# Optimization experiments

Measured on AMD Instinct MI355X. Metric: run time of the kernel, lower is better.

The kernel has to match this reference:

```python
import jax, jax.numpy as jnp
from jax import lax
import numpy as np

DN = ('NCHW', 'OIHW', 'NCHW')

def _conv(x, w, b, s, p):
    out = lax.conv_general_dilated(x, w, (s, s), ((p, p), (p, p)), dimension_numbers=DN)
    return out + b[None, :, None, None]

def _convt(x, w, b):
    # torch ConvTranspose2d(k=3, stride=2, pad=1, out_pad=1) == lhs-dilated conv
    # with flipped kernel, pad (k-1-p, k-1-p+op) = (1, 2). Doubles H, W.
    wk = jnp.flip(w, (2, 3)).transpose(1, 0, 2, 3)  # [Cin,Cout,k,k] -> [Cout,Cin,k,k]
    out = lax.conv_general_dilated(x, wk, (1, 1), ((1, 2), (1, 2)), lhs_dilation=(2, 2), dimension_numbers=DN)
    return out + b[None, :, None, None]

def _bn(x, g, b):
    # training-mode batch stats over (N, H, W), eps=1e-5
    m = jnp.mean(x, (0, 2, 3), keepdims=True)
    v = jnp.var(x, (0, 2, 3), keepdims=True)
    return (x - m) * lax.rsqrt(v + 1e-5) * g[None, :, None, None] + b[None, :, None, None]

def _hsw(x):
    return x * jnp.clip(x + 3.0, 0.0, 6.0) * (1.0 / 6.0)

SCORE_THRESHOLD = 0.6
DOWN_SCALE = 4.0

def _forward(feature, ch_w1, ch_b1, ch_w2, ch_b2, ch_w3, ch_b3, ch_g1, ch_be1, ch_g2, ch_be2,
             cl_w1, cl_b1, cl_w2, cl_b2, cl_g, cl_be, cl_dw, cl_db,
             rg_tw, rg_tb, rg_g, rg_be, rg_w, rg_b, hm_tw, hm_tb):
    # ---- CommonHead (note: original reuses bn1 after both stride-2 convs) ----
    h = _bn(_conv(feature, ch_w1, ch_b1, 2, 1), ch_g1, ch_be1)   # [B,192,64,64]
    h = _bn(_conv(h, ch_w2, ch_b2, 2, 1), ch_g1, ch_be1)         # [B,192,32,32]
    h = _hsw(_bn(_conv(h, ch_w3, ch_b3, 1, 0), ch_g2, ch_be2))   # [B,32,32,32]
    # ---- PageClassifyNet ----
    c = _hsw(_bn(_conv(h, cl_w1, cl_b1, 1, 1), cl_g, cl_be))     # [B,32,32,32]
    c = _conv(c, cl_w2, cl_b2, 1, 1)                             # [B,1,32,32]
    cls = c.reshape(c.shape[0], -1) @ cl_dw.T + cl_db            # [B,2]
    r = _hsw(_bn(_convt(feature, rg_tw, rg_tb), rg_g, rg_be))    # [B,32,256,256]
    reg = _conv(r, rg_w, rg_b, 1, 1)                             # [B,2,256,256]
    # ---- AuxiliaryHeatmapNet ----
    hm = _convt(feature, hm_tw, hm_tb)                           # [B,8,256,256]
    # ---- keypoint decode (threshold + argmax + gather), vectorized over batch ----
    B, _, H, W = hm.shape
    flat = hm.transpose(0, 2, 3, 1).reshape(B, H * W, 8)          # HWC layout as in source
    pages = jnp.stack([flat[..., :4], flat[..., 4:]], axis=1)     # [B,2(pages),HW,4(corners)]
    idx = jnp.argmax(pages, axis=2)                               # [B,2,4] flat spatial index
    y_idx = (idx // W).astype(reg.dtype)
    x_idx = (idx % W).astype(reg.dtype)
    fi = idx.reshape(B, -1)                                       # [B,8]
    reg_flat = reg.reshape(B, 2, H * W)
    off_x = jnp.take_along_axis(reg_flat[:, 0, :], fi, axis=1).reshape(B, 2, 4)
    off_y = jnp.take_along_axis(reg_flat[:, 1, :], fi, axis=1).reshape(B, 2, 4)
    xs = jnp.clip((off_x + x_idx) * DOWN_SCALE / (W * DOWN_SCALE), 0.0, 1.0)
    ys = jnp.clip((off_y + y_idx) * DOWN_SCALE / (H * DOWN_SCALE), 0.0, 1.0)
    valid = cls > SCORE_THRESHOLD                                 # [B,2]
    label = jnp.broadcast_to(jnp.arange(2, dtype=xs.dtype)[None, :], (B, 2))
    row = jnp.concatenate([label[..., None], xs, ys], axis=-1)    # [B,2,9]
    return jnp.where(valid[..., None], row, jnp.asarray(-1.0, xs.dtype))


def setup_inputs() -> dict:
    key = jax.random.key(0)
    ks = jax.random.split(key, 32)
    rn = lambda k, shp, s=0.05: jax.random.normal(k, shp, dtype=jnp.float32) * s
    d = {}
    d['feature'] = jax.random.normal(ks[0], (8, 512, 128, 128), dtype=jnp.float32)
    d['ch_w1'] = rn(ks[1], (192, 512, 3, 3)); d['ch_b1'] = rn(ks[2], (192,))
    d['ch_w2'] = rn(ks[3], (192, 192, 3, 3)); d['ch_b2'] = rn(ks[4], (192,))
    d['ch_w3'] = rn(ks[5], (32, 192, 1, 1)); d['ch_b3'] = rn(ks[6], (32,))
    d['ch_g1'] = jnp.ones((192,), jnp.float32); d['ch_be1'] = jnp.zeros((192,), jnp.float32)
    d['ch_g2'] = jnp.ones((32,), jnp.float32); d['ch_be2'] = jnp.zeros((32,), jnp.float32)
    d['cl_w1'] = rn(ks[7], (32, 32, 3, 3)); d['cl_b1'] = rn(ks[8], (32,))
    d['cl_w2'] = rn(ks[9], (1, 32, 3, 3)); d['cl_b2'] = rn(ks[10], (1,))
    d['cl_g'] = jnp.ones((32,), jnp.float32); d['cl_be'] = jnp.zeros((32,), jnp.float32)
    d['cl_dw'] = rn(ks[11], (2, 1024), 0.1); d['cl_db'] = rn(ks[12], (2,))
    d['rg_tw'] = rn(ks[13], (512, 32, 3, 3)); d['rg_tb'] = rn(ks[14], (32,))
    d['rg_g'] = jnp.ones((32,), jnp.float32); d['rg_be'] = jnp.zeros((32,), jnp.float32)
    d['rg_w'] = rn(ks[15], (2, 32, 3, 3)); d['rg_b'] = rn(ks[16], (2,))
    d['hm_tw'] = rn(ks[17], (512, 8, 3, 3)); d['hm_tb'] = rn(ks[18], (8,))
    return d


def reference(feature, ch_w1, ch_b1, ch_w2, ch_b2, ch_w3, ch_b3, ch_g1, ch_be1, ch_g2, ch_be2,
              cl_w1, cl_b1, cl_w2, cl_b2, cl_g, cl_be, cl_dw, cl_db,
              rg_tw, rg_tb, rg_g, rg_be, rg_w, rg_b, hm_tw, hm_tb):
    return _forward(feature, ch_w1, ch_b1, ch_w2, ch_b2, ch_w3, ch_b3, ch_g1, ch_be1, ch_g2, ch_be2,
                    cl_w1, cl_b1, cl_w2, cl_b2, cl_g, cl_be, cl_dw, cl_db,
                    rg_tw, rg_tb, rg_g, rg_be, rg_w, rg_b, hm_tw, hm_tb)
```

## Files before the change

### kernel.cpp

```cpp
#include <hip/hip_runtime.h>

typedef unsigned short u16;
typedef u16 u16x8 __attribute__((ext_vector_type(8)));
typedef __bf16 bf16x8 __attribute__((ext_vector_type(8)));
typedef float f32x4 __attribute__((ext_vector_type(4)));

__device__ __forceinline__ float bf2f(u16 v) {
  unsigned u = ((unsigned)v) << 16;
  return __builtin_bit_cast(float, u);
}
__device__ __forceinline__ u16 f2bf(float f) {
  unsigned u = __builtin_bit_cast(unsigned, f);
  u += 0x7FFFu + ((u >> 16) & 1u);
  return (u16)(u >> 16);
}
__device__ __forceinline__ float hsw(float v) {
  return v * fminf(fmaxf(v + 3.f, 0.f), 6.f) * (1.f / 6.f);
}
__device__ __forceinline__ f32x4 mfma16(u16x8 a, u16x8 b, f32x4 c) {
  return __builtin_amdgcn_mfma_f32_16x16x32_bf16(
      __builtin_bit_cast(bf16x8, a), __builtin_bit_cast(bf16x8, b), c, 0, 0, 0);
}

#define LR 40

__global__ __launch_bounds__(256) void k_tobf(const float* __restrict__ f,
                                              u16* __restrict__ fbh) {
  __shared__ float tl[64 * 65];
  const int t = threadIdx.x;
  const int bid = blockIdx.x;
  const int ict = bid & 7, xt = (bid >> 3) & 1, y = (bid >> 4) & 127, n = bid >> 11;
  const int x0 = xt * 64, ic0 = ict * 64;
#pragma unroll
  for (int i = 0; i < 16; ++i) {
    const int e = t + i * 256;
    const int icl = e >> 6, xl = e & 63;
    tl[icl * 65 + xl] = f[((n * 512 + ic0 + icl) * 128 + y) * 128 + x0 + xl];
  }
  __syncthreads();
#pragma unroll
  for (int i = 0; i < 16; ++i) {
    const int e = t + i * 256;
    const int xl = e >> 6, icl = e & 63;
    const size_t idx = ((size_t)((n * 128 + y) * 128 + x0 + xl) << 9) + ic0 + icl;
    fbh[idx] = f2bf(tl[icl * 65 + xl]);
  }
}

__global__ __launch_bounds__(256) void k_pack1(const float* __restrict__ w,
                                               u16* __restrict__ bph) {
  const int e = blockIdx.x * 256 + threadIdx.x;
  const int ici = e & 31;
  const int rest = e >> 5;
  const int oc = rest % 192;
  const int kc = rest / 192;
  const int icc = kc & 15, tap = kc >> 4;
  const int ic = icc * 32 + ici;
  bph[e] = f2bf(w[(oc * 512 + ic) * 9 + tap]);
}

__global__ __launch_bounds__(256) void k_pack2(const float* __restrict__ w,
                                               u16* __restrict__ bph) {
  const int e = blockIdx.x * 256 + threadIdx.x;
  const int ici = e & 31;
  const int rest = e >> 5;
  const int oc = rest % 192;
  const int kc = rest / 192;
  const int icc = kc % 6, tap = kc / 6;
  const int ic = icc * 32 + ici;
  bph[e] = f2bf(w[(oc * 192 + ic) * 9 + tap]);
}

__global__ __launch_bounds__(256) void k_pack5(const float* __restrict__ rgw,
                                               const float* __restrict__ hmw,
                                               u16* __restrict__ bph) {
  const int e = blockIdx.x * 256 + threadIdx.x;
  const int ici = e & 31;
  const int rest = e >> 5;
  const int oc = rest % 48;
  const int sic = rest / 48;
  const int icc = sic & 15, slot = sic >> 4;
  const int ic = icc * 32 + ici;
  const int kytab[9] = {1, 1, 1, 2, 0, 2, 2, 0, 0};
  const int kxtab[9] = {1, 2, 0, 1, 1, 2, 0, 2, 0};
  const int ky = kytab[slot], kx = kxtab[slot];
  float v = 0.f;
  if (oc < 32)
    v = rgw[((ic * 32 + oc) * 3 + ky) * 3 + kx];
  else if (oc < 40)
    v = hmw[((ic * 8 + (oc - 32)) * 3 + ky) * 3 + kx];
  bph[e] = f2bf(v);
}

__global__ __launch_bounds__(256) void k_conv1(const u16* __restrict__ fbh,
                                               const u16* __restrict__ bph,
                                               const float* __restrict__ bias,
                                               u16* __restrict__ y1) {
  __shared__ u16 Al[64 * LR];
  __shared__ u16 Bl[192 * LR];
  __shared__ float bl[192];
  const int t = threadIdx.x;
  const int n = blockIdx.x >> 6, oy = blockIdx.x & 63;
  if (t < 192) bl[t] = bias[t];
  const int lane = t & 63, wv = t >> 6;
  const int row = lane & 15, g = lane >> 4;
  const int oxs = t >> 2, icq = t & 3;
  const f32x4 z4 = {0.f, 0.f, 0.f, 0.f};
  f32x4 acc[4][3];
#pragma unroll
  for (int i = 0; i < 4; ++i)
#pragma unroll
    for (int j = 0; j < 3; ++j) acc[i][j] = z4;

#define C1_LOAD(KC, AV, BV)                                                    \
  {                                                                            \
    const int tap_ = (KC) >> 4, icc_ = (KC)&15;                                \
    const int ky_ = tap_ / 3, kx_ = tap_ - ky_ * 3;                            \
    const int iy_ = 2 * oy - 1 + ky_;                                          \
    const int ix_ = 2 * oxs - 1 + kx_;                                         \
    u16x8 v_ = {0, 0, 0, 0, 0, 0, 0, 0};                                       \
    if ((unsigned)iy_ < 128u && (unsigned)ix_ < 128u)                          \
      v_ = *(const u16x8*)&fbh[((size_t)((n * 128 + iy_) * 128 + ix_) << 9) +  \
                               icc_ * 32 + icq * 8];                           \
    AV = v_;                                                                   \
    const size_t bbase_ = (size_t)(tap_ * 16 + icc_) * (192 * 32);             \
    _Pragma("unroll") for (int i_ = 0; i_ < 3; ++i_) {                         \
      const int e_ = t + i_ * 256;                                             \
      BV[i_] = *(const u16x8*)&bph[bbase_ + (e_ >> 2) * 32 + (e_ & 3) * 8];    \
    }                                                                          \
  }

  u16x8 avA, bvA[3], avB, bvB[3];
  C1_LOAD(0, avA, bvA);

  for (int kc = 0; kc < 144; ++kc) {
    __syncthreads();
    *(u16x8*)&Al[oxs * LR + icq * 8] = avA;
#pragma unroll
    for (int i = 0; i < 3; ++i) {
      const int e = t + i * 256;
      *(u16x8*)&Bl[(e >> 2) * LR + (e & 3) * 8] = bvA[i];
    }
    __syncthreads();
    if (kc < 143) C1_LOAD(kc + 1, avB, bvB);
    u16x8 af[4], bf[3];
#pragma unroll
    for (int mf = 0; mf < 4; ++mf)
      af[mf] = *(const u16x8*)&Al[(mf * 16 + row) * LR + g * 8];
#pragma unroll
    for (int nf = 0; nf < 3; ++nf)
      bf[nf] = *(const u16x8*)&Bl[(wv * 48 + nf * 16 + row) * LR + g * 8];
#pragma unroll
    for (int mf = 0; mf < 4; ++mf)
#pragma unroll
      for (int nf = 0; nf < 3; ++nf) acc[mf][nf] = mfma16(af[mf], bf[nf], acc[mf][nf]);
    avA = avB;
#pragma unroll
    for (int i = 0; i < 3; ++i) bvA[i] = bvB[i];
  }
#undef C1_LOAD
#pragma unroll
  for (int mf = 0; mf < 4; ++mf)
#pragma unroll
    for (int nf = 0; nf < 3; ++nf)
#pragma unroll
      for (int r = 0; r < 4; ++r) {
        const int m = mf * 16 + g * 4 + r;
        const int oc = wv * 48 + nf * 16 + row;
        y1[((n * 64 + oy) * 64 + m) * 192 + oc] = f2bf(acc[mf][nf][r] + bl[oc]);
      }
}

__global__ __launch_bounds__(256) void k_conv2(const u16* __restrict__ y1,
                                               const u16* __restrict__ bph,
                                               const float* __restrict__ bias,
                                               const float* __restrict__ sc,
                                               const float* __restrict__ sh,
                                               float* __restrict__ y2) {
  __shared__ u16 Al[64 * LR];
  __shared__ u16 Bl[192 * LR];
  __shared__ float bl[192], scl[192], shl[192];
  const int t = threadIdx.x;
  const int n = blockIdx.x >> 4, oyp = blockIdx.x & 15;
  if (t < 192) {
    bl[t] = bias[t];
    scl[t] = sc[t];
    shl[t] = sh[t];
  }
  __syncthreads();
  const int lane = t & 63, wv = t >> 6;
  const int row = lane & 15, g = lane >> 4;
  const int ms = t >> 2, icq = t & 3;
  const int ryr = ms >> 5, oxs = ms & 31;
  const f32x4 z4 = {0.f, 0.f, 0.f, 0.f};
  f32x4 acc[4][3];
#pragma unroll
  for (int i = 0; i < 4; ++i)
#pragma unroll
    for (int j = 0; j < 3; ++j) acc[i][j] = z4;

#define C2_LOAD(KC, RAW, OK, BV)                                               \
  {                                                                            \
    const int tap_ = (KC) / 6, icc_ = (KC)-tap_ * 6;                           \
    const int ky_ = tap_ / 3, kx_ = tap_ - ky_ * 3;                            \
    const int iy_ = 2 * (oyp * 2 + ryr) - 1 + ky_;                             \
    const int ix_ = 2 * oxs - 1 + kx_;                                         \
    OK = ((unsigned)iy_ < 64u) && ((unsigned)ix_ < 64u);                       \
    u16x8 v_ = {0, 0, 0, 0, 0, 0, 0, 0};                                       \
    if (OK)                                                                    \
      v_ = *(const u16x8*)&y1[((n * 64 + iy_) * 64 + ix_) * 192 + icc_ * 32 +  \
                              icq * 8];                                        \
    RAW = v_;                                                                  \
    const size_t bbase_ = (size_t)(tap_ * 6 + icc_) * (192 * 32);              \
    _Pragma("unroll") for (int i_ = 0; i_ < 3; ++i_) {                         \
      const int e_ = t + i_ * 256;                                             \
      BV[i_] = *(const u16x8*)&bph[bbase_ + (e_ >> 2) * 32 + (e_ & 3) * 8];    \
    }                                                                          \
  }

  u16x8 rawA, bvA[3], rawB, bvB[3];
  bool okA, okB;
  C2_LOAD(0, rawA, okA, bvA);

  for (int kc = 0; kc < 54; ++kc) {
    const int tap = kc / 6, icc = kc - tap * 6;
    const int icb = icc * 32 + icq * 8;
    u16x8 av = {0, 0, 0, 0, 0, 0, 0, 0};
    if (okA) {
#pragma unroll
      for (int j = 0; j < 8; ++j)
        av[j] = f2bf(bf2f(rawA[j]) * scl[icb + j] + shl[icb + j]);
    }
    __syncthreads();
    *(u16x8*)&Al[ms * LR + icq * 8] = av;
#pragma unroll
    for (int i = 0; i < 3; ++i) {
      const int e = t + i * 256;
      *(u16x8*)&Bl[(e >> 2) * LR + (e & 3) * 8] = bvA[i];
    }
    __syncthreads();
    if (kc < 53) C2_LOAD(kc + 1, rawB, okB, bvB);
    u16x8 af[4], bf[3];
#pragma unroll
    for (int mf = 0; mf < 4; ++mf)
      af[mf] = *(const u16x8*)&Al[(mf * 16 + row) * LR + g * 8];
#pragma unroll
    for (int nf = 0; nf < 3; ++nf)
      bf[nf] = *(const u16x8*)&Bl[(wv * 48 + nf * 16 + row) * LR + g * 8];
#pragma unroll
    for (int mf = 0; mf < 4; ++mf)
#pragma unroll
      for (int nf = 0; nf < 3; ++nf) acc[mf][nf] = mfma16(af[mf], bf[nf], acc[mf][nf]);
    rawA = rawB;
    okA = okB;
#pragma unroll
    for (int i = 0; i < 3; ++i) bvA[i] = bvB[i];
  }
#undef C2_LOAD
#pragma unroll
  for (int mf = 0; mf < 4; ++mf)
#pragma unroll
    for (int nf = 0; nf < 3; ++nf)
#pragma unroll
      for (int r = 0; r < 4; ++r) {
        const int m = mf * 16 + g * 4 + r;
        const int oy = oyp * 2 + (m >> 5), ox = m & 31;
        const int oc = wv * 48 + nf * 16 + row;
        y2[((n * 32 + oy) * 32 + ox) * 192 + oc] = acc[mf][nf][r] + bl[oc];
      }
}

#define AST2 32
#define ARS2 (129 * 32)
__global__ __launch_bounds__(256) void k_convt(const u16* __restrict__ fbh,
                                               const u16* __restrict__ bph,
                                               const float* __restrict__ rgb,
                                               const float* __restrict__ hmb,
                                               u16* __restrict__ rr,
                                               float* __restrict__ hm) {
  __shared__ u16 AH[2 * ARS2];
  __shared__ u16 BH[9 * 48 * 32];
  const int t = threadIdx.x;
  const int bid = (blockIdx.x & 7) * 128 + (blockIdx.x >> 3);
  const int n = bid >> 7, iyb = bid & 127;
  const int lane = t & 63, wv = t >> 6;
  const int row = lane & 15, g = lane >> 4;

  if (t < 8) {
    const int r = t >> 2, j = t & 3;
    const u16x8 z = {0, 0, 0, 0, 0, 0, 0, 0};
    *(u16x8*)&AH[r * ARS2 + 128 * AST2 + j * 8] = z;
  }

  float bias3[3];
#pragma unroll
  for (int nf = 0; nf < 3; ++nf) {
    const int oc = nf * 16 + row;
    bias3[nf] = (oc < 32) ? rgb[oc] : ((oc < 40) ? hmb[oc - 32] : 0.f);
  }

  const int SCt[9] = {0, 1, 1, 2, 2, 3, 3, 3, 3};
  const int SDt[9] = {0, 0, 0, 0, 1, 0, 0, 1, 1};
  const int SXt[9] = {0, 0, 1, 0, 0, 0, 1, 0, 1};

  int rr_[4], px_[4], iq_[4];
#pragma unroll
  for (int i = 0; i < 4; ++i) {
    const int u = t + i * 256;
    rr_[i] = u >> 9;
    px_[i] = (u >> 2) & 127;
    iq_[i] = u & 3;
  }

  const f32x4 z4 = {0.f, 0.f, 0.f, 0.f};
  f32x4 acc[4][2][3];
#pragma unroll
  for (int c = 0; c < 4; ++c)
#pragma unroll
    for (int m = 0; m < 2; ++m)
#pragma unroll
      for (int j = 0; j < 3; ++j) acc[c][m][j] = z4;

#define LOAD_A(ICC, DST)                                                       \
  _Pragma("unroll") for (int i = 0; i < 4; ++i) {                              \
    const int iy = iyb + rr_[i];                                               \
    u16x8 v = {0, 0, 0, 0, 0, 0, 0, 0};                                        \
    if (iy < 128)                                                              \
      v = *(const u16x8*)&fbh[((size_t)((n * 128 + iy) * 128 + px_[i]) << 9) + \
                              (ICC)*32 + iq_[i] * 8];                          \
    DST[i] = v;                                                                \
  }

#define LOAD_B(ICC, DST)                                                       \
  _Pragma("unroll") for (int i = 0; i < 7; ++i) {                              \
    const int e = t + i * 256;                                                 \
    u16x8 v = {0, 0, 0, 0, 0, 0, 0, 0};                                        \
    if (e < 1728) {                                                            \
      const int slot = e / 192, rem = e % 192;                                 \
      const int oc = rem >> 2, icq = rem & 3;                                  \
      v = *(const u16x8*)&bph[((size_t)((slot * 16 + (ICC)) * 48 + oc) << 5) + \
                              icq * 8];                                        \
    }                                                                          \
    DST[i] = v;                                                                \
  }

  u16x8 ahA[4], bhA[7], ahB[4], bhB[7];
  LOAD_A(0, ahA);
  LOAD_B(0, bhA);

  for (int icc = 0; icc < 16; ++icc) {
    __syncthreads();
#pragma unroll
    for (int i = 0; i < 4; ++i)
      *(u16x8*)&AH[rr_[i] * ARS2 + px_[i] * AST2 + iq_[i] * 8] = ahA[i];
#pragma unroll
    for (int i = 0; i < 7; ++i) {
      const int e = t + i * 256;
      if (e < 1728) {
        const int slot = e / 192, rem = e % 192;
        const int oc = rem >> 2, icq = rem & 3;
        *(u16x8*)&BH[(slot * 48 + oc) * AST2 + icq * 8] = bhA[i];
      }
    }
    __syncthreads();

    if (icc < 15) {
      LOAD_A(icc + 1, ahB);
      LOAD_B(icc + 1, bhB);
    }

    u16x8 afr[2][2][2];
#pragma unroll
    for (int diy = 0; diy < 2; ++diy)
#pragma unroll
      for (int mfl = 0; mfl < 2; ++mfl)
#pragma unroll
        for (int dix = 0; dix < 2; ++dix)
          afr[diy][mfl][dix] =
              *(const u16x8*)&AH[diy * ARS2 +
                                 ((wv * 2 + mfl) * 16 + row + dix) * AST2 + g * 8];

#pragma unroll
    for (int slot = 0; slot < 9; ++slot) {
      const int cls = SCt[slot], diy = SDt[slot], dix = SXt[slot];
      const u16x8 bf0 = *(const u16x8*)&BH[(slot * 48 + row) * AST2 + g * 8];
      const u16x8 bf1 = *(const u16x8*)&BH[(slot * 48 + 16 + row) * AST2 + g * 8];
      const u16x8 bf2 = *(const u16x8*)&BH[(slot * 48 + 32 + row) * AST2 + g * 8];
#pragma unroll
      for (int mfl = 0; mfl < 2; ++mfl) {
        const u16x8 af = afr[diy][mfl][dix];
        acc[cls][mfl][0] = mfma16(af, bf0, acc[cls][mfl][0]);
        acc[cls][mfl][1] = mfma16(af, bf1, acc[cls][mfl][1]);
        acc[cls][mfl][2] = mfma16(af, bf2, acc[cls][mfl][2]);
      }
    }

#pragma unroll
    for (int i = 0; i < 4; ++i) ahA[i] = ahB[i];
#pragma unroll
    for (int i = 0; i < 7; ++i) bhA[i] = bhB[i];
  }
#undef LOAD_A
#undef LOAD_B

#pragma unroll
  for (int cls = 0; cls < 4; ++cls) {
    const int oy = 2 * iyb + (cls >> 1);
    const int xp = cls & 1;
#pragma unroll
    for (int mfl = 0; mfl < 2; ++mfl)
#pragma unroll
      for (int nf = 0; nf < 3; ++nf)
#pragma unroll
        for (int r = 0; r < 4; ++r) {
          const int m = (wv * 2 + mfl) * 16 + g * 4 + r;
          const int ox = 2 * m + xp;
          const int oc = nf * 16 + row;
          const float v = acc[cls][mfl][nf][r] + bias3[nf];
          if (oc < 32)
            rr[((size_t)((n * 256 + oy) * 256 + ox)) * 32 + oc] = f2bf(v);
          else if (oc < 40)
            hm[(size_t)(n * 8 + (oc - 32)) * 65536 + oy * 256 + ox] = v;
        }
  }
}

template <int CG, bool BF16>
__global__ __launch_bounds__(256) void k_stats(const void* __restrict__ in_, int M,
                                               int PB, float* __restrict__ gsum,
                                               float* __restrict__ gsq) {
  const int C = CG * 32;
  __shared__ float red[8][CG * 32];
  const int t = threadIdx.x;
  const int pg = t >> 5, ln = t & 31;
  float s[CG], q[CG];
#pragma unroll
  for (int c = 0; c < CG; ++c) { s[c] = 0.f; q[c] = 0.f; }
  const int p0 = blockIdx.x * PB;
  const int pend = min(p0 + PB, M);
  for (int p = p0 + pg; p < pend; p += 8) {
#pragma unroll
    for (int c = 0; c < CG; ++c) {
      float v;
      if (BF16)
        v = bf2f(((const u16*)in_)[(size_t)p * C + c * 32 + ln]);
      else
        v = ((const float*)in_)[(size_t)p * C + c * 32 + ln];
      s[c] += v;
      q[c] += v * v;
    }
  }
#pragma unroll
  for (int c = 0; c < CG; ++c) red[pg][c * 32 + ln] = s[c];
  __syncthreads();
  if (t < C) {
    float tot = 0.f;
#pragma unroll
    for (int k = 0; k < 8; ++k) tot += red[k][t];
    atomicAdd(&gsum[t], tot);
  }
  __syncthreads();
#pragma unroll
  for (int c = 0; c < CG; ++c) red[pg][c * 32 + ln] = q[c];
  __syncthreads();
  if (t < C) {
    float tot = 0.f;
#pragma unroll
    for (int k = 0; k < 8; ++k) tot += red[k][t];
    atomicAdd(&gsq[t], tot);
  }
}

__global__ void k_bnfin(const float* __restrict__ gsum, const float* __restrict__ gsq,
                        const float* __restrict__ g, const float* __restrict__ be,
                        float invM, int C, float* __restrict__ sc,
                        float* __restrict__ sh) {
  const int t = threadIdx.x;
  if (t < C) {
    const float m = gsum[t] * invM;
    const float var = gsq[t] * invM - m * m;
    const float inv = rsqrtf(var + 1e-5f);
    const float s = g[t] * inv;
    sc[t] = s;
    sh[t] = be[t] - m * s;
  }
}

__global__ __launch_bounds__(256) void k_conv3(const float* __restrict__ y2,
                                               const float* __restrict__ w3,
                                               const float* __restrict__ b3,
                                               const float* __restrict__ sc,
                                               const float* __restrict__ sh,
                                               float* __restrict__ y3) {
  __shared__ float wl[32 * 192];
  __shared__ float scl[192], shl[192];
  const int t = threadIdx.x;
  for (int e = t; e < 6144; e += 256) wl[e] = w3[e];
  if (t < 192) {
    scl[t] = sc[t];
    shl[t] = sh[t];
  }
  __syncthreads();
  const int px = blockIdx.x * 256 + t;
  float acc[32];
#pragma unroll
  for (int oc = 0; oc < 32; ++oc) acc[oc] = 0.f;
  const float* base = &y2[(size_t)px * 192];
  for (int icb = 0; icb < 192; icb += 8) {
    const f32x4 r0 = *(const f32x4*)&base[icb];
    const f32x4 r1 = *(const f32x4*)&base[icb + 4];
    float v[8];
#pragma unroll
    for (int j = 0; j < 8; ++j) {
      const float r = (j < 4) ? r0[j & 3] : r1[j & 3];
      v[j] = r * scl[icb + j] + shl[icb + j];
    }
#pragma unroll
    for (int oc = 0; oc < 32; ++oc) {
      const f32x4 w0 = *(const f32x4*)&wl[oc * 192 + icb];
      const f32x4 w1 = *(const f32x4*)&wl[oc * 192 + icb + 4];
      acc[oc] += v[0] * w0[0] + v[1] * w0[1] + v[2] * w0[2] + v[3] * w0[3] +
                 v[4] * w1[0] + v[5] * w1[1] + v[6] * w1[2] + v[7] * w1[3];
    }
  }
#pragma unroll
  for (int oc = 0; oc < 32; ++oc) y3[(size_t)px * 32 + oc] = acc[oc] + b3[oc];
}

__global__ __launch_bounds__(256) void k_clsconv1(const float* __restrict__ y3,
                                                  const float* __restrict__ w1,
                                                  const float* __restrict__ b1,
                                                  const float* __restrict__ sc,
                                                  const float* __restrict__ sh,
                                                  float* __restrict__ c1) {
  __shared__ float wl[9216];
  __shared__ float scl[32], shl[32];
  const int t = threadIdx.x;
  for (int e = t; e < 9216; e += 256) {
    const int oc = e & 31;
    const int tmp = e >> 5;
    const int tap = tmp % 9, ic = tmp / 9;
    wl[e] = w1[(oc * 32 + ic) * 9 + tap];
  }
  if (t < 32) {
    scl[t] = sc[t];
    shl[t] = sh[t];
  }
  __syncthreads();
  const int px = blockIdx.x * 64 + (t & 63);
  const int ocg = t >> 6;
  const int n = px >> 10, y0 = (px >> 5) & 31, x0 = px & 31;
  float acc[8];
#pragma unroll
  for (int j = 0; j < 8; ++j) acc[j] = 0.f;
  for (int tap = 0; tap < 9; ++tap) {
    const int dy = tap / 3 - 1, dx = tap % 3 - 1;
    const int yy = y0 + dy, xx = x0 + dx;
    if ((unsigned)yy < 32u && (unsigned)xx < 32u) {
      const float* ib = &y3[((n << 10) + yy * 32 + xx) * 32];
      for (int ic = 0; ic < 32; ++ic) {
        const float v = hsw(ib[ic] * scl[ic] + shl[ic]);
        const float* wp = &wl[(ic * 9 + tap) * 32 + ocg * 8];
#pragma unroll
        for (int j = 0; j < 8; ++j) acc[j] += v * wp[j];
      }
    }
  }
#pragma unroll
  for (int j = 0; j < 8; ++j) c1[px * 32 + ocg * 8 + j] = acc[j] + b1[ocg * 8 + j];
}

__global__ __launch_bounds__(256) void k_cls(const float* __restrict__ c1,
                                             const float* __restrict__ w2,
                                             const float* __restrict__ b2,
                                             const float* __restrict__ dw,
                                             const float* __restrict__ db,
                                             const float* __restrict__ sc,
                                             const float* __restrict__ sh,
                                             float* __restrict__ cls) {
  __shared__ float wl[288];
  __shared__ float scl[32], shl[32];
  __shared__ float red0[256], red1[256];
  const int t = threadIdx.x;
  const int n = blockIdx.x;
  for (int e = t; e < 288; e += 256) wl[e] = w2[e];
  if (t < 32) {
    scl[t] = sc[t];
    shl[t] = sh[t];
  }
  __syncthreads();
  float s0 = 0.f, s1 = 0.f;
  for (int i = 0; i < 4; ++i) {
    const int px = i * 256 + t;
    const int y0 = px >> 5, x0 = px & 31;
    float c2 = b2[0];
    for (int tap = 0; tap < 9; ++tap) {
      const int dy = tap / 3 - 1, dx = tap % 3 - 1;
      const int yy = y0 + dy, xx = x0 + dx;
      if ((unsigned)yy < 32u && (unsigned)xx < 32u) {
        const float* ib = &c1[((n << 10) + yy * 32 + xx) * 32];
        for (int ic = 0; ic < 32; ++ic)
          c2 += hsw(ib[ic] * scl[ic] + shl[ic]) * wl[ic * 9 + tap];
      }
    }
    s0 += c2 * dw[px];
    s1 += c2 * dw[1024 + px];
  }
  red0[t] = s0;
  red1[t] = s1;
  __syncthreads();
  for (int s = 128; s; s >>= 1) {
    if (t < s) {
      red0[t] += red0[t + s];
      red1[t] += red1[t + s];
    }
    __syncthreads();
  }
  if (t == 0) {
    cls[n * 2 + 0] = red0[0] + db[0];
    cls[n * 2 + 1] = red1[0] + db[1];
  }
}

__global__ __launch_bounds__(256) void k_regconv(const u16* __restrict__ rr,
                                                 const float* __restrict__ w,
                                                 const float* __restrict__ b,
                                                 const float* __restrict__ sc,
                                                 const float* __restrict__ sh,
                                                 float* __restrict__ reg) {
  __shared__ u16 rl[3 * 258 * 33];
  __shared__ float wl[576];
  __shared__ float scl[32], shl[32];
  const int t = threadIdx.x;
  const int n = blockIdx.x >> 8, oy = blockIdx.x & 255;
  for (int e = t; e < 576; e += 256) wl[e] = w[e];
  if (t < 32) {
    scl[t] = sc[t];
    shl[t] = sh[t];
  }
  if (t < 192) {
    const int ry = t / 64, side = (t >> 5) & 1, ic = t & 31;
    rl[(ry * 258 + side * 257) * 33 + ic] = 0;
  }
  __syncthreads();
  for (int e = t; e < 3072; e += 256) {
    const int icq8 = e & 3;
    const int pxx = (e >> 2) & 255;
    const int ry = e >> 10;
    const int rowi = oy - 1 + ry;
    u16x8 raw = {0, 0, 0, 0, 0, 0, 0, 0};
    bool ok = (unsigned)rowi < 256u;
    if (ok)
      raw = *(const u16x8*)&rr[((size_t)((n * 256 + rowi) * 256 + pxx)) * 32 + icq8 * 8];
#pragma unroll
    for (int j = 0; j < 8; ++j) {
      const int ic = icq8 * 8 + j;
      float v = 0.f;
      if (ok) v = hsw(bf2f(raw[j]) * scl[ic] + shl[ic]);
      rl[(ry * 258 + pxx + 1) * 33 + ic] = f2bf(v);
    }
  }
  __syncthreads();
  const int px = t;
  float a0 = b[0], a1 = b[1];
#pragma unroll
  for (int ry = 0; ry < 3; ++ry)
#pragma unroll
    for (int kx = 0; kx < 3; ++kx) {
      const u16* ib = &rl[(ry * 258 + px + kx) * 33];
      for (int ic = 0; ic < 32; ++ic) {
        const float v = bf2f(ib[ic]);
        a0 += v * wl[ic * 9 + ry * 3 + kx];
        a1 += v * wl[288 + ic * 9 + ry * 3 + kx];
      }
    }
  reg[(n * 2 + 0) * 65536 + oy * 256 + px] = a0;
  reg[(n * 2 + 1) * 65536 + oy * 256 + px] = a1;
}

__global__ __launch_bounds__(256) void k_argmax(const float* __restrict__ hm,
                                                int* __restrict__ idx) {
  __shared__ float bv[256];
  __shared__ int bi[256];
  const int t = threadIdx.x;
  const float* base = &hm[(size_t)blockIdx.x * 65536];
  float best = -3.402823466e38f;
  int bidx = 2147483647;
  for (int i = t; i < 65536; i += 256) {
    const float v = base[i];
    if (v > best) {
      best = v;
      bidx = i;
    }
  }
  bv[t] = best;
  bi[t] = bidx;
  __syncthreads();
  for (int s = 128; s; s >>= 1) {
    if (t < s) {
      if (bv[t + s] > bv[t] || (bv[t + s] == bv[t] && bi[t + s] < bi[t])) {
        bv[t] = bv[t + s];
        bi[t] = bi[t + s];
      }
    }
    __syncthreads();
  }
  if (t == 0) idx[blockIdx.x] = bi[0];
}

__global__ void k_final(const float* __restrict__ cls, const int* __restrict__ idx,
                        const float* __restrict__ reg, float* __restrict__ out) {
  const int t = threadIdx.x;
  if (t >= 16) return;
  const int n = t >> 1, p = t & 1;
  const float cv = cls[n * 2 + p];
  float* o = &out[(n * 2 + p) * 9];
  if (!(cv > 0.6f)) {
    for (int i = 0; i < 9; ++i) o[i] = -1.f;
    return;
  }
  o[0] = (float)p;
  for (int c = 0; c < 4; ++c) {
    const int id = idx[n * 8 + p * 4 + c];
    const int yi = id >> 8, xi = id & 255;
    const float ox_ = reg[(n * 2 + 0) * 65536 + id];
    const float oy_ = reg[(n * 2 + 1) * 65536 + id];
    o[1 + c] = fminf(fmaxf((ox_ + (float)xi) * (1.f / 256.f), 0.f), 1.f);
    o[5 + c] = fminf(fmaxf((oy_ + (float)yi) * (1.f / 256.f), 0.f), 1.f);
  }
}

extern "C" void kernel_launch(void* const* d_in, const int* in_sizes, int n_in,
                              void* d_out, int out_size, void* d_ws, size_t ws_size,
                              hipStream_t stream) {
  const float* feature = (const float*)d_in[0];
  const float* ch_w1 = (const float*)d_in[1];
  const float* ch_b1 = (const float*)d_in[2];
  const float* ch_w2 = (const float*)d_in[3];
  const float* ch_b2 = (const float*)d_in[4];
  const float* ch_w3 = (const float*)d_in[5];
  const float* ch_b3 = (const float*)d_in[6];
  const float* ch_g1 = (const float*)d_in[7];
  const float* ch_be1 = (const float*)d_in[8];
  const float* ch_g2 = (const float*)d_in[9];
  const float* ch_be2 = (const float*)d_in[10];
  const float* cl_w1 = (const float*)d_in[11];
  const float* cl_b1 = (const float*)d_in[12];
  const float* cl_w2 = (const float*)d_in[13];
  const float* cl_b2 = (const float*)d_in[14];
  const float* cl_g = (const float*)d_in[15];
  const float* cl_be = (const float*)d_in[16];
  const float* cl_dw = (const float*)d_in[17];
  const float* cl_db = (const float*)d_in[18];
  const float* rg_tw = (const float*)d_in[19];
  const float* rg_tb = (const float*)d_in[20];
  const float* rg_g = (const float*)d_in[21];
  const float* rg_be = (const float*)d_in[22];
  const float* rg_w = (const float*)d_in[23];
  const float* rg_b = (const float*)d_in[24];
  const float* hm_tw = (const float*)d_in[25];
  const float* hm_tb = (const float*)d_in[26];
  float* out = (float*)d_out;

  char* w = (char*)d_ws;
  const size_t OFF_FB = 0;
  const size_t OFF_BP1 = 134217728;
  const size_t OFF_BP2 = 135987200;
  const size_t OFF_BP5 = 136650752;
  const size_t OFF_Y1 = 137093120;
  const size_t OFF_Y2 = 149676032;
  const size_t OFF_Y3 = 155967488;
  const size_t OFF_C1 = 157016064;
  const size_t OFF_RR = 158064640;
  const size_t OFF_HM = 191619072;
  const size_t OFF_REG = 208396288;
  const size_t OFF_STATS = 212590592;
  const size_t OFF_PARAMS = 212594432;
  const size_t OFF_CLS = 212598272;
  const size_t OFF_IDX = 212598336;
  const size_t WS_NEED = 212598592;
  if (ws_size < WS_NEED) return;

  u16* FB = (u16*)(w + OFF_FB);
  u16* BP1 = (u16*)(w + OFF_BP1);
  u16* BP2 = (u16*)(w + OFF_BP2);
  u16* BP5 = (u16*)(w + OFF_BP5);
  u16* Y1 = (u16*)(w + OFF_Y1);
  float* Y2 = (float*)(w + OFF_Y2);
  float* Y3 = (float*)(w + OFF_Y3);
  float* C1 = (float*)(w + OFF_C1);
  u16* RR = (u16*)(w + OFF_RR);
  float* HM = (float*)(w + OFF_HM);
  float* REG = (float*)(w + OFF_REG);
  float* GSUM = (float*)(w + OFF_STATS);
  float* GSQ = GSUM + 480;
  float* SC = (float*)(w + OFF_PARAMS);
  float* SH = SC + 480;
  float* CLS = (float*)(w + OFF_CLS);
  int* IDX = (int*)(w + OFF_IDX);

  (void)hipMemsetAsync(w + OFF_STATS, 0, 3840, stream);

  k_tobf<<<16384, 256, 0, stream>>>(feature, FB);
  k_pack1<<<3456, 256, 0, stream>>>(ch_w1, BP1);
  k_pack2<<<1296, 256, 0, stream>>>(ch_w2, BP2);
  k_pack5<<<864, 256, 0, stream>>>(rg_tw, hm_tw, BP5);

  k_conv1<<<512, 256, 0, stream>>>(FB, BP1, ch_b1, Y1);
  k_stats<6, true><<<128, 256, 0, stream>>>(Y1, 32768, 256, GSUM + 0, GSQ + 0);
  k_bnfin<<<1, 256, 0, stream>>>(GSUM + 0, GSQ + 0, ch_g1, ch_be1, 1.f / 32768.f, 192,
                                 SC + 0, SH + 0);
  k_conv2<<<128, 256, 0, stream>>>(Y1, BP2, ch_b2, SC + 0, SH + 0, Y2);
  k_stats<6, false><<<32, 256, 0, stream>>>(Y2, 8192, 256, GSUM + 192, GSQ + 192);
  k_bnfin<<<1, 256, 0, stream>>>(GSUM + 192, GSQ + 192, ch_g1, ch_be1, 1.f / 8192.f,
                                 192, SC + 192, SH + 192);
  k_conv3<<<32, 256, 0, stream>>>(Y2, ch_w3, ch_b3, SC + 192, SH + 192, Y3);
  k_stats<1, false><<<8, 256, 0, stream>>>(Y3, 8192, 1024, GSUM + 384, GSQ + 384);
  k_bnfin<<<1, 256, 0, stream>>>(GSUM + 384, GSQ + 384, ch_g2, ch_be2, 1.f / 8192.f,
                                 32, SC + 384, SH + 384);
  k_clsconv1<<<128, 256, 0, stream>>>(Y3, cl_w1, cl_b1, SC + 384, SH + 384, C1);
  k_stats<1, false><<<8, 256, 0, stream>>>(C1, 8192, 1024, GSUM + 416, GSQ + 416);
  k_bnfin<<<1, 256, 0, stream>>>(GSUM + 416, GSQ + 416, cl_g, cl_be, 1.f / 8192.f, 32,
                                 SC + 416, SH + 416);
  k_cls<<<8, 256, 0, stream>>>(C1, cl_w2, cl_b2, cl_dw, cl_db, SC + 416, SH + 416,
                               CLS);
  k_convt<<<1024, 256, 0, stream>>>(FB, BP5, rg_tb, hm_tb, RR, HM);
  k_stats<1, true><<<256, 256, 0, stream>>>(RR, 524288, 2048, GSUM + 448, GSQ + 448);
  k_bnfin<<<1, 256, 0, stream>>>(GSUM + 448, GSQ + 448, rg_g, rg_be, 1.f / 524288.f,
                                 32, SC + 448, SH + 448);
  k_regconv<<<2048, 256, 0, stream>>>(RR, rg_w, rg_b, SC + 448, SH + 448, REG);
  k_argmax<<<64, 256, 0, stream>>>(HM, IDX);
  k_final<<<1, 64, 0, stream>>>(CLS, IDX, REG, out);
}
```

Before: 849.5 us.

## Restructure conv1 to stage 3-row input halo per channel chunk across all taps

conv1 now stages a 3-row by 130-pixel input strip and all 9 taps of weights for one 32-channel chunk in LDS, iterating 16 chunks instead of 144 tap-chunks. The output channels are split into 4 groups, launching four times as many blocks. This cuts barrier count and reuses each input tile across taps. It also pads the convt LDS row strides to 40 to avoid bank conflicts, and loads A fragments inside the slot loop instead of preloading them, which lowers register pressure. The cost is more LDS per block and redundant input loads across the 4 channel-group blocks.

```diff
diff --git a/kernel.cpp b/kernel.cpp
--- a/kernel.cpp
+++ b/kernel.cpp
@@ -96,79 +96,112 @@
                                                const u16* __restrict__ bph,
                                                const float* __restrict__ bias,
                                                u16* __restrict__ y1) {
-  __shared__ u16 Al[64 * LR];
-  __shared__ u16 Bl[192 * LR];
-  __shared__ float bl[192];
-  const int t = threadIdx.x;
-  const int n = blockIdx.x >> 6, oy = blockIdx.x & 63;
-  if (t < 192) bl[t] = bias[t];
+  __shared__ u16 AL[3 * 130 * LR];
+  __shared__ u16 BH[9 * 48 * LR];
+  const int t = threadIdx.x;
+  const int bid = blockIdx.x;
+  const int ocg = bid & 3, oy = (bid >> 2) & 63, n = bid >> 8;
   const int lane = t & 63, wv = t >> 6;
   const int row = lane & 15, g = lane >> 4;
-  const int oxs = t >> 2, icq = t & 3;
+
+  float bias3[3];
+#pragma unroll
+  for (int nf = 0; nf < 3; ++nf) bias3[nf] = bias[ocg * 48 + nf * 16 + row];
+
   const f32x4 z4 = {0.f, 0.f, 0.f, 0.f};
-  f32x4 acc[4][3];
-#pragma unroll
-  for (int i = 0; i < 4; ++i)
-#pragma unroll
-    for (int j = 0; j < 3; ++j) acc[i][j] = z4;
-
-#define C1_LOAD(KC, AV, BV)                                                    \
-  {                                                                            \
-    const int tap_ = (KC) >> 4, icc_ = (KC)&15;                                \
-    const int ky_ = tap_ / 3, kx_ = tap_ - ky_ * 3;                            \
-    const int iy_ = 2 * oy - 1 + ky_;                                          \
-    const int ix_ = 2 * oxs - 1 + kx_;                                         \
-    u16x8 v_ = {0, 0, 0, 0, 0, 0, 0, 0};                                       \
-    if ((unsigned)iy_ < 128u && (unsigned)ix_ < 128u)                          \
-      v_ = *(const u16x8*)&fbh[((size_t)((n * 128 + iy_) * 128 + ix_) << 9) +  \
-                               icc_ * 32 + icq * 8];                           \
-    AV = v_;                                                                   \
-    const size_t bbase_ = (size_t)(tap_ * 16 + icc_) * (192 * 32);             \
-    _Pragma("unroll") for (int i_ = 0; i_ < 3; ++i_) {                         \
-      const int e_ = t + i_ * 256;                                             \
-      BV[i_] = *(const u16x8*)&bph[bbase_ + (e_ >> 2) * 32 + (e_ & 3) * 8];    \
+  f32x4 acc[3];
+#pragma unroll
+  for (int j = 0; j < 3; ++j) acc[j] = z4;
+
+#define C1_LOAD_A(ICC, DST)                                                    \
+  _Pragma("unroll") for (int i = 0; i < 7; ++i) {                              \
+    const int e = t + i * 256;                                                 \
+    u16x8 v = {0, 0, 0, 0, 0, 0, 0, 0};                                        \
+    if (e < 1560) {                                                            \
+      const int icq = e & 3, q = e >> 2;                                       \
+      const int ry = q / 130, p = q - ry * 130;                                \
+      const int iy = 2 * oy - 1 + ry, ix = p - 1;                              \
+      if (iy >= 0 && (unsigned)ix < 128u)                                      \
+        v = *(const u16x8*)&fbh[((size_t)((n * 128 + iy) * 128 + ix) << 9) +   \
+                                (ICC)*32 + icq * 8];                           \
     }                                                                          \
-  }
-
-  u16x8 avA, bvA[3], avB, bvB[3];
-  C1_LOAD(0, avA, bvA);
-
-  for (int kc = 0; kc < 144; ++kc) {
+    DST[i] = v;                                                                \
+  }
+
+#define C1_LOAD_B(ICC, DST)                                                    \
+  _Pragma("unroll") for (int i = 0; i < 7; ++i) {                              \
+    const int e = t + i * 256;                                                 \
+    u16x8 v = {0, 0, 0, 0, 0, 0, 0, 0};                                        \
+    if (e < 1728) {                                                            \
+      const int icq = e & 3, q = e >> 2;                                       \
+      const int tap = q / 48, oco = q - tap * 48;                              \
+      v = *(const u16x8*)&bph[((size_t)((tap * 16 + (ICC)) * 192 + ocg * 48 +  \
+                                        oco)                                   \
+                              << 5) +                                          \
+                              icq * 8];                                        \
+    }                                                                          \
+    DST[i] = v;                                                                \
+  }
+
+  u16x8 aA[7], bA[7], aB[7], bB[7];
+  C1_LOAD_A(0, aA);
+  C1_LOAD_B(0, bA);
+
+  for (int icc = 0; icc < 16; ++icc) {
     __syncthreads();
-    *(u16x8*)&Al[oxs * LR + icq * 8] = avA;
-#pragma unroll
-    for (int i = 0; i < 3; ++i) {
+#pragma unroll
+    for (int i = 0; i < 7; ++i) {
       const int e = t + i * 256;
-      *(u16x8*)&Bl[(e >> 2) * LR + (e & 3) * 8] = bvA[i];
+      if (e < 1560) {
+        const int icq = e & 3, q = e >> 2;
+        *(u16x8*)&AL[q * LR + icq * 8] = aA[i];
+      }
+    }
+#pragma unroll
+    for (int i = 0; i < 7; ++i) {
+      const int e = t + i * 256;
+      if (e < 1728) {
+        const int icq = e & 3, q = e >> 2;
+        *(u16x8*)&BH[q * LR + icq * 8] = bA[i];
+      }
     }
     __syncthreads();
-    if (kc < 143) C1_LOAD(kc + 1, avB, bvB);
-    u16x8 af[4], bf[3];
-#pragma unroll
-    for (int mf = 0; mf < 4; ++mf)
-      af[mf] = *(const u16x8*)&Al[(mf * 16 + row) * LR + g * 8];
-#pragma unroll
-    for (int nf = 0; nf < 3; ++nf)
-      bf[nf] = *(const u16x8*)&Bl[(wv * 48 + nf * 16 + row) * LR + g * 8];
-#pragma unroll
-    for (int mf = 0; mf < 4; ++mf)
-#pragma unroll
-      for (int nf = 0; nf < 3; ++nf) acc[mf][nf] = mfma16(af[mf], bf[nf], acc[mf][nf]);
-    avA = avB;
-#pragma unroll
-    for (int i = 0; i < 3; ++i) bvA[i] = bvB[i];
-  }
-#undef C1_LOAD
-#pragma unroll
-  for (int mf = 0; mf < 4; ++mf)
-#pragma unroll
-    for (int nf = 0; nf < 3; ++nf)
-#pragma unroll
-      for (int r = 0; r < 4; ++r) {
-        const int m = mf * 16 + g * 4 + r;
-        const int oc = wv * 48 + nf * 16 + row;
-        y1[((n * 64 + oy) * 64 + m) * 192 + oc] = f2bf(acc[mf][nf][r] + bl[oc]);
-      }
+
+    if (icc < 15) {
+      C1_LOAD_A(icc + 1, aB);
+      C1_LOAD_B(icc + 1, bB);
+    }
+
+#pragma unroll
+    for (int tap = 0; tap < 9; ++tap) {
+      const int ry = tap / 3, kx = tap - ry * 3;
+      const int p = 2 * (wv * 16 + row) + kx;
+      const u16x8 af = *(const u16x8*)&AL[(ry * 130 + p) * LR + g * 8];
+      const u16x8 bf0 = *(const u16x8*)&BH[(tap * 48 + row) * LR + g * 8];
+      const u16x8 bf1 = *(const u16x8*)&BH[(tap * 48 + 16 + row) * LR + g * 8];
+      const u16x8 bf2 = *(const u16x8*)&BH[(tap * 48 + 32 + row) * LR + g * 8];
+      acc[0] = mfma16(af, bf0, acc[0]);
+      acc[1] = mfma16(af, bf1, acc[1]);
+      acc[2] = mfma16(af, bf2, acc[2]);
+    }
+
+#pragma unroll
+    for (int i = 0; i < 7; ++i) {
+      aA[i] = aB[i];
+      bA[i] = bB[i];
+    }
+  }
+#undef C1_LOAD_A
+#undef C1_LOAD_B
+
+#pragma unroll
+  for (int nf = 0; nf < 3; ++nf)
+#pragma unroll
+    for (int r = 0; r < 4; ++r) {
+      const int m = wv * 16 + g * 4 + r;
+      const int oc = ocg * 48 + nf * 16 + row;
+      y1[((n * 64 + oy) * 64 + m) * 192 + oc] = f2bf(acc[nf][r] + bias3[nf]);
+    }
 }
 
 __global__ __launch_bounds__(256) void k_conv2(const u16* __restrict__ y1,
@@ -270,16 +303,17 @@
       }
 }
 
-#define AST2 32
-#define ARS2 (129 * 32)
+#define AST 40
+#define ARS (130 * 40)
+#define BST 40
 __global__ __launch_bounds__(256) void k_convt(const u16* __restrict__ fbh,
                                                const u16* __restrict__ bph,
                                                const float* __restrict__ rgb,
                                                const float* __restrict__ hmb,
                                                u16* __restrict__ rr,
                                                float* __restrict__ hm) {
-  __shared__ u16 AH[2 * ARS2];
-  __shared__ u16 BH[9 * 48 * 32];
+  __shared__ u16 AH[2 * ARS];
+  __shared__ u16 BH[9 * 48 * BST];
   const int t = threadIdx.x;
   const int bid = (blockIdx.x & 7) * 128 + (blockIdx.x >> 3);
   const int n = bid >> 7, iyb = bid & 127;
@@ -289,7 +323,7 @@
   if (t < 8) {
     const int r = t >> 2, j = t & 3;
     const u16x8 z = {0, 0, 0, 0, 0, 0, 0, 0};
-    *(u16x8*)&AH[r * ARS2 + 128 * AST2 + j * 8] = z;
+    *(u16x8*)&AH[r * ARS + 128 * AST + j * 8] = z;
   }
 
   float bias3[3];
@@ -352,14 +386,14 @@
     __syncthreads();
 #pragma unroll
     for (int i = 0; i < 4; ++i)
-      *(u16x8*)&AH[rr_[i] * ARS2 + px_[i] * AST2 + iq_[i] * 8] = ahA[i];
+      *(u16x8*)&AH[rr_[i] * ARS + px_[i] * AST + iq_[i] * 8] = ahA[i];
 #pragma unroll
     for (int i = 0; i < 7; ++i) {
       const int e = t + i * 256;
       if (e < 1728) {
         const int slot = e / 192, rem = e % 192;
         const int oc = rem >> 2, icq = rem & 3;
-        *(u16x8*)&BH[(slot * 48 + oc) * AST2 + icq * 8] = bhA[i];
+        *(u16x8*)&BH[(slot * 48 + oc) * BST + icq * 8] = bhA[i];
       }
     }
     __syncthreads();
@@ -369,26 +403,17 @@
       LOAD_B(icc + 1, bhB);
     }
 
-    u16x8 afr[2][2][2];
-#pragma unroll
-    for (int diy = 0; diy < 2; ++diy)
-#pragma unroll
-      for (int mfl = 0; mfl < 2; ++mfl)
-#pragma unroll
-        for (int dix = 0; dix < 2; ++dix)
-          afr[diy][mfl][dix] =
-              *(const u16x8*)&AH[diy * ARS2 +
-                                 ((wv * 2 + mfl) * 16 + row + dix) * AST2 + g * 8];
-
 #pragma unroll
     for (int slot = 0; slot < 9; ++slot) {
       const int cls = SCt[slot], diy = SDt[slot], dix = SXt[slot];
-      const u16x8 bf0 = *(const u16x8*)&BH[(slot * 48 + row) * AST2 + g * 8];
-      const u16x8 bf1 = *(const u16x8*)&BH[(slot * 48 + 16 + row) * AST2 + g * 8];
-      const u16x8 bf2 = *(const u16x8*)&BH[(slot * 48 + 32 + row) * AST2 + g * 8];
+      const u16x8 bf0 = *(const u16x8*)&BH[(slot * 48 + row) * BST + g * 8];
+      const u16x8 bf1 = *(const u16x8*)&BH[(slot * 48 + 16 + row) * BST + g * 8];
+      const u16x8 bf2 = *(const u16x8*)&BH[(slot * 48 + 32 + row) * BST + g * 8];
 #pragma unroll
       for (int mfl = 0; mfl < 2; ++mfl) {
-        const u16x8 af = afr[diy][mfl][dix];
+        const int mf = wv * 2 + mfl;
+        const u16x8 af =
+            *(const u16x8*)&AH[diy * ARS + (mf * 16 + row + dix) * AST + g * 8];
         acc[cls][mfl][0] = mfma16(af, bf0, acc[cls][mfl][0]);
         acc[cls][mfl][1] = mfma16(af, bf1, acc[cls][mfl][1]);
         acc[cls][mfl][2] = mfma16(af, bf2, acc[cls][mfl][2]);
@@ -806,7 +831,7 @@
   k_pack2<<<1296, 256, 0, stream>>>(ch_w2, BP2);
   k_pack5<<<864, 256, 0, stream>>>(rg_tw, hm_tw, BP5);
 
-  k_conv1<<<512, 256, 0, stream>>>(FB, BP1, ch_b1, Y1);
+  k_conv1<<<2048, 256, 0, stream>>>(FB, BP1, ch_b1, Y1);
   k_stats<6, true><<<128, 256, 0, stream>>>(Y1, 32768, 256, GSUM + 0, GSQ + 0);
   k_bnfin<<<1, 256, 0, stream>>>(GSUM + 0, GSQ + 0, ch_g1, ch_be1, 1.f / 32768.f, 192,
                                  SC + 0, SH + 0);
```

Result: slower. 874.7 us (+3.0%).
